# Performance work log

Measured on AMD Instinct MI355X. Metric: run time of the kernel, lower is better.

## Reference

```python
import jax, jax.numpy as jnp
import numpy as np
import math

EMB = 128
N_HEADS = 8
HEAD_DIM = EMB // N_HEADS
TANH_CLIP = 10.0
NEG_INF = -1e9


def make_heads(x, n_heads):
    # x: (B, n, H) -> (B, n_heads, n, head_dim)
    B, n, H = x.shape
    return x.reshape(B, n, n_heads, H // n_heads).transpose(0, 2, 1, 3)


def setup_inputs() -> dict:
    key = jax.random.key(0)
    ks = jax.random.split(key, 11)
    B, N, H = 64, 2000, EMB
    s = 1.0 / math.sqrt(H)
    return {
        "patch_embeddings": jax.random.normal(ks[0], (B, N, H), jnp.float32),
        "fixed_content_cls": jax.random.normal(ks[1], (B, 1, H), jnp.float32),
        "Wq_graph": jax.random.normal(ks[2], (H, H), jnp.float32) * s,
        "Wq_first": jax.random.normal(ks[3], (H, H), jnp.float32) * s,
        "Wq_last": jax.random.normal(ks[4], (H, H), jnp.float32) * s,
        "Wk": jax.random.normal(ks[5], (H, H), jnp.float32) * s,
        "Wv": jax.random.normal(ks[6], (H, H), jnp.float32) * s,
        "logit_Wk": jax.random.normal(ks[7], (H, H), jnp.float32) * s,
        "Wc": jax.random.normal(ks[8], (H, H), jnp.float32) * s,
        "bc": jax.random.normal(ks[9], (H,), jnp.float32) * s,
        "last_patch": jax.random.randint(ks[10], (B,), 0, N, jnp.int64),
    }


def reference(patch_embeddings, fixed_content_cls, Wq_graph, Wq_first, Wq_last,
              Wk, Wv, logit_Wk, Wc, bc, last_patch):
    B, N, H = patch_embeddings.shape
    bidx = jnp.arange(B)

    # reset(): precomputed projections over all patches (memory-dominant)
    q_graph = make_heads(fixed_content_cls @ Wq_graph.T, N_HEADS)   # (B, nh, 1, hd)
    glimpse_k = make_heads(patch_embeddings @ Wk.T, N_HEADS)        # (B, nh, N, hd)
    glimpse_v = make_heads(patch_embeddings @ Wv.T, N_HEADS)        # (B, nh, N, hd)
    logit_k = patch_embeddings @ logit_Wk.T                          # (B, N, H)

    # mask the just-visited patch (emulate -inf with large negative for stability)
    mask = jnp.zeros((B, N), patch_embeddings.dtype).at[bidx, last_patch].set(NEG_INF)

    # gather last patch embedding: (B, 1, H)
    last_emb = patch_embeddings[bidx, last_patch][:, None, :]
    q_first = make_heads(last_emb @ Wq_first.T, N_HEADS)
    q_last = make_heads(last_emb @ Wq_last.T, N_HEADS)
    glimpse_q = q_graph + q_first + q_last                          # (B, nh, 1, hd)

    # masked multi-head attention, q_len = 1
    scores = jnp.einsum('bhqd,bhnd->bhqn', glimpse_q, glimpse_k) / math.sqrt(HEAD_DIM)
    scores = scores + mask[:, None, None, :]
    attn = jax.nn.softmax(scores, axis=-1)
    out = jnp.einsum('bhqn,bhnd->bhqd', attn, glimpse_v)            # (B, nh, 1, hd)
    out = out.transpose(0, 2, 1, 3).reshape(B, 1, H)

    final_q = out @ Wc.T + bc                                        # (B, 1, H)

    # tanh-clipped pointer logits over all N patches
    score = jnp.einsum('bqh,bnh->bqn', final_q, logit_k) / math.sqrt(H)  # (B, 1, N)
    score_masked = TANH_CLIP * jnp.tanh(score[:, 0, :]) + mask          # (B, N)
    probs = jax.nn.softmax(score_masked, axis=1)
    return probs
```

## Files before the change

kernel.cpp:

```cpp
#include <hip/hip_runtime.h>
#include <math.h>

#define BB 64
#define NN 2000
#define HH 128
#define NHEAD 8
#define SP 8

__global__ __launch_bounds__(128) void k1_prep(
    const float* __restrict__ pe, const float* __restrict__ cls,
    const float* __restrict__ Wqg, const float* __restrict__ Wqf,
    const float* __restrict__ Wql, const float* __restrict__ Wk,
    const int* __restrict__ lp, float* __restrict__ qk_out) {
  __shared__ float4 sc4[32], sl4[32];
  __shared__ float q[HH];
  int b = blockIdx.x, t = threadIdx.x;
  int last = lp[b];
  if (t < 32) {
    sc4[t] = ((const float4*)(cls + b*HH))[t];
    sl4[t] = ((const float4*)(pe + ((long)b*NN + last)*HH))[t];
  }
  __syncthreads();
  const float4* wg = (const float4*)(Wqg + t*HH);
  const float4* wf = (const float4*)(Wqf + t*HH);
  const float4* wl = (const float4*)(Wql + t*HH);
  float acc = 0.f;
  #pragma unroll 8
  for (int j = 0; j < 32; j++) {
    float4 g = wg[j], f = wf[j], l = wl[j], c = sc4[j], s = sl4[j];
    acc += g.x*c.x + g.y*c.y + g.z*c.z + g.w*c.w;
    acc += (f.x+l.x)*s.x + (f.y+l.y)*s.y + (f.z+l.z)*s.z + (f.w+l.w)*s.w;
  }
  q[t] = acc;
  __syncthreads();
  #pragma unroll
  for (int h = 0; h < NHEAD; h++) {
    float a = 0.f;
    #pragma unroll
    for (int d = 0; d < 16; d++)
      a += q[h*16+d] * Wk[(h*16+d)*HH + t];
    qk_out[(b*NHEAD + h)*HH + t] = a * 0.25f;
  }
}

__global__ __launch_bounds__(256) void k2a_scores(
    const float* __restrict__ pe, const float* __restrict__ qk,
    const int* __restrict__ lp, float* __restrict__ pout) {
  int b = blockIdx.y, sp = blockIdx.x, tid = threadIdx.x;
  int n = sp*256 + tid;
  int nc = min(n, NN-1);
  const float4* prow = (const float4*)(pe + ((long)b*NN + nc)*HH);
  const float4* qk4  = (const float4*)(qk + (long)b*NHEAD*HH);
  float d[NHEAD];
  #pragma unroll
  for (int h = 0; h < NHEAD; h++) d[h] = 0.f;
  #pragma unroll 2
  for (int j = 0; j < 32; j += 4) {
    float4 v0 = prow[j], v1 = prow[j+1], v2 = prow[j+2], v3 = prow[j+3];
    #pragma unroll
    for (int h = 0; h < NHEAD; h++) {
      float4 q0 = qk4[h*32+j], q1 = qk4[h*32+j+1];
      float4 q2 = qk4[h*32+j+2], q3 = qk4[h*32+j+3];
      d[h] += v0.x*q0.x + v0.y*q0.y + v0.z*q0.z + v0.w*q0.w
            + v1.x*q1.x + v1.y*q1.y + v1.z*q1.z + v1.w*q1.w
            + v2.x*q2.x + v2.y*q2.y + v2.z*q2.z + v2.w*q2.w
            + v3.x*q3.x + v3.y*q3.y + v3.z*q3.z + v3.w*q3.w;
    }
  }
  int last = lp[b];
  bool live = (n < NN) && (n != last);
  float4 p0, p1;
  p0.x = live ? __expf(d[0]) : 0.f;
  p0.y = live ? __expf(d[1]) : 0.f;
  p0.z = live ? __expf(d[2]) : 0.f;
  p0.w = live ? __expf(d[3]) : 0.f;
  p1.x = live ? __expf(d[4]) : 0.f;
  p1.y = live ? __expf(d[5]) : 0.f;
  p1.z = live ? __expf(d[6]) : 0.f;
  p1.w = live ? __expf(d[7]) : 0.f;
  if (n < NN) {
    float4* po = (float4*)(pout + ((long)b*NN + n)*NHEAD);
    po[0] = p0; po[1] = p1;
  }
}

__global__ __launch_bounds__(256) void k2b_wsum(
    const float* __restrict__ pe, const float* __restrict__ pin,
    float* __restrict__ Wpart, float* __restrict__ lpart) {
  int b = blockIdx.y, sp = blockIdx.x, tid = threadIdx.x;
  int w = tid >> 6, lane = tid & 63;
  __shared__ float4 pst[4][128];
  __shared__ float4 wred[NHEAD][4][32];
  __shared__ float lred[4][NHEAD];
  int chunk = sp*256 + w*64;
  const float4* pin4 = (const float4*)pin;
  {
    float4 z = make_float4(0.f,0.f,0.f,0.f);
    int k0 = lane, k1 = lane + 64;
    int n0 = chunk + (k0 >> 1), n1 = chunk + (k1 >> 1);
    pst[w][k0] = (n0 < NN) ? pin4[((long)b*NN + n0)*2 + (k0&1)] : z;
    pst[w][k1] = (n1 < NN) ? pin4[((long)b*NN + n1)*2 + (k1&1)] : z;
  }
  __syncthreads();
  int rhalf = lane >> 5, j4 = lane & 31;
  const float4* peg = (const float4*)pe;
  float4 wa[NHEAD];
  float la[NHEAD];
  #pragma unroll
  for (int h = 0; h < NHEAD; h++) { wa[h] = make_float4(0.f,0.f,0.f,0.f); la[h] = 0.f; }
  for (int i = 0; i < 32; i++) {
    int nl = i*2 + rhalf;
    int ng = chunk + nl;
    float4 v = peg[((long)b*NN + min(ng, NN-1))*32 + j4];
    float4 pa = pst[w][nl*2], pb = pst[w][nl*2+1];
    wa[0].x += pa.x*v.x; wa[0].y += pa.x*v.y; wa[0].z += pa.x*v.z; wa[0].w += pa.x*v.w; la[0] += pa.x;
    wa[1].x += pa.y*v.x; wa[1].y += pa.y*v.y; wa[1].z += pa.y*v.z; wa[1].w += pa.y*v.w; la[1] += pa.y;
    wa[2].x += pa.z*v.x; wa[2].y += pa.z*v.y; wa[2].z += pa.z*v.z; wa[2].w += pa.z*v.w; la[2] += pa.z;
    wa[3].x += pa.w*v.x; wa[3].y += pa.w*v.y; wa[3].z += pa.w*v.z; wa[3].w += pa.w*v.w; la[3] += pa.w;
    wa[4].x += pb.x*v.x; wa[4].y += pb.x*v.y; wa[4].z += pb.x*v.z; wa[4].w += pb.x*v.w; la[4] += pb.x;
    wa[5].x += pb.y*v.x; wa[5].y += pb.y*v.y; wa[5].z += pb.y*v.z; wa[5].w += pb.y*v.w; la[5] += pb.y;
    wa[6].x += pb.z*v.x; wa[6].y += pb.z*v.y; wa[6].z += pb.z*v.z; wa[6].w += pb.z*v.w; la[6] += pb.z;
    wa[7].x += pb.w*v.x; wa[7].y += pb.w*v.y; wa[7].z += pb.w*v.z; wa[7].w += pb.w*v.w; la[7] += pb.w;
  }
  #pragma unroll
  for (int h = 0; h < NHEAD; h++) {
    wa[h].x += __shfl_xor(wa[h].x, 32);
    wa[h].y += __shfl_xor(wa[h].y, 32);
    wa[h].z += __shfl_xor(wa[h].z, 32);
    wa[h].w += __shfl_xor(wa[h].w, 32);
    la[h]   += __shfl_xor(la[h], 32);
  }
  if (lane < 32) {
    #pragma unroll
    for (int h = 0; h < NHEAD; h++) wred[h][w][lane] = wa[h];
  }
  if (lane == 0) {
    #pragma unroll
    for (int h = 0; h < NHEAD; h++) lred[w][h] = la[h];
  }
  __syncthreads();
  int h2 = tid >> 5, c = tid & 31;
  float4 s0 = wred[h2][0][c], s1 = wred[h2][1][c], s2 = wred[h2][2][c], s3 = wred[h2][3][c];
  float4 s;
  s.x = s0.x + s1.x + s2.x + s3.x;
  s.y = s0.y + s1.y + s2.y + s3.y;
  s.z = s0.z + s1.z + s2.z + s3.z;
  s.w = s0.w + s1.w + s2.w + s3.w;
  ((float4*)(Wpart + ((long)(b*SP + sp)*NHEAD + h2)*HH))[c] = s;
  if (tid < NHEAD)
    lpart[(b*SP + sp)*NHEAD + tid] =
        lred[0][tid] + lred[1][tid] + lred[2][tid] + lred[3][tid];
}

__global__ __launch_bounds__(256) void k34(
    const float* __restrict__ lpart, const float* __restrict__ Wpart,
    const float* __restrict__ Wv, const float* __restrict__ Wc,
    const float* __restrict__ bc, const float* __restrict__ lWk,
    float* __restrict__ lq_out) {
  int b = blockIdx.x, tid = threadIdx.x;
  __shared__ float Wns[NHEAD*HH];
  __shared__ float ls[NHEAD];
  __shared__ float tmp[2][HH];
  __shared__ float outf[HH], fq[HH];
  for (int e = tid; e < NHEAD*HH; e += 256) {
    float a = 0.f;
    #pragma unroll
    for (int s = 0; s < SP; s++) a += Wpart[((long)(b*SP+s)*NHEAD)*HH + e];
    Wns[e] = a;
  }
  if (tid < NHEAD) {
    float l = 0.f;
    #pragma unroll
    for (int s = 0; s < SP; s++) l += lpart[(b*SP+s)*NHEAD + tid];
    ls[tid] = l;
  }
  __syncthreads();
  int t = tid & 127, half = tid >> 7;
  {
    int h = t >> 4;
    const float4* wv = (const float4*)(Wv + t*HH);
    const float4* wn = (const float4*)(Wns + h*HH);
    float a = 0.f;
    #pragma unroll 4
    for (int j = half*16; j < half*16 + 16; j++) {
      float4 v = wv[j], nn = wn[j];
      a += v.x*nn.x + v.y*nn.y + v.z*nn.z + v.w*nn.w;
    }
    tmp[half][t] = a;
    __syncthreads();
    if (half == 0) outf[t] = (tmp[0][t] + tmp[1][t]) / ls[t>>4];
    __syncthreads();
  }
  {
    const float4* wc = (const float4*)(Wc + t*HH);
    const float4* of = (const float4*)outf;
    float a = 0.f;
    #pragma unroll 4
    for (int k = half*16; k < half*16 + 16; k++) {
      float4 v = wc[k], nn = of[k];
      a += v.x*nn.x + v.y*nn.y + v.z*nn.z + v.w*nn.w;
    }
    tmp[half][t] = a;
    __syncthreads();
    if (half == 0) fq[t] = tmp[0][t] + tmp[1][t] + bc[t];
    __syncthreads();
  }
  {
    float a = 0.f;
    #pragma unroll 4
    for (int i = half*64; i < half*64 + 64; i++)
      a += fq[i] * lWk[i*HH + t];
    tmp[half][t] = a;
    __syncthreads();
    if (half == 0)
      lq_out[b*HH + t] = (tmp[0][t] + tmp[1][t]) * 0.08838834764831845f;
  }
}

__global__ __launch_bounds__(256) void k4_logits(
    const float* __restrict__ pe, const float* __restrict__ lq,
    const int* __restrict__ lp, float* __restrict__ eout, float* __restrict__ psum) {
  int b = blockIdx.y, sp = blockIdx.x, tid = threadIdx.x;
  int n = sp*256 + tid;
  int nc = min(n, NN-1);
  const float4* prow = (const float4*)(pe + ((long)b*NN + nc)*HH);
  const float4* lq4  = (const float4*)(lq + (long)b*HH);
  float a0 = 0.f, a1 = 0.f, a2 = 0.f, a3 = 0.f;
  #pragma unroll 2
  for (int j = 0; j < 32; j += 4) {
    float4 v0 = prow[j], v1 = prow[j+1], v2 = prow[j+2], v3 = prow[j+3];
    float4 q0 = lq4[j], q1 = lq4[j+1], q2 = lq4[j+2], q3 = lq4[j+3];
    a0 += v0.x*q0.x + v0.y*q0.y + v0.z*q0.z + v0.w*q0.w;
    a1 += v1.x*q1.x + v1.y*q1.y + v1.z*q1.z + v1.w*q1.w;
    a2 += v2.x*q2.x + v2.y*q2.y + v2.z*q2.z + v2.w*q2.w;
    a3 += v3.x*q3.x + v3.y*q3.y + v3.z*q3.z + v3.w*q3.w;
  }
  float acc = (a0 + a1) + (a2 + a3);
  int last = lp[b];
  float e = (n < NN && n != last) ? __expf(-20.f / (__expf(2.f*acc) + 1.f)) : 0.f;
  if (n < NN) eout[b*NN + n] = e;
  float s = e;
  #pragma unroll
  for (int d = 1; d < 64; d <<= 1) s += __shfl_xor(s, d);
  __shared__ float red[4];
  if ((tid & 63) == 0) red[tid >> 6] = s;
  __syncthreads();
  if (tid == 0) psum[b*SP + sp] = red[0] + red[1] + red[2] + red[3];
}

__global__ __launch_bounds__(256) void k5_scale(
    const float* __restrict__ eout, const float* __restrict__ psum,
    float* __restrict__ out) {
  int b = blockIdx.y, sp = blockIdx.x, tid = threadIdx.x;
  __shared__ float S;
  if (tid == 0) {
    float a = 0.f;
    #pragma unroll
    for (int s = 0; s < SP; s++) a += psum[b*SP + s];
    S = a;
  }
  __syncthreads();
  float inv = 1.f / S;
  int lo = sp*250;
  int n = lo + tid;
  if (tid < 250) out[b*NN + n] = eout[b*NN + n] * inv;
}

extern "C" void kernel_launch(void* const* d_in, const int* in_sizes, int n_in,
                              void* d_out, int out_size, void* d_ws, size_t ws_size,
                              hipStream_t stream) {
  (void)in_sizes; (void)n_in; (void)out_size; (void)ws_size;
  const float* pe   = (const float*)d_in[0];
  const float* cls  = (const float*)d_in[1];
  const float* Wqg  = (const float*)d_in[2];
  const float* Wqf  = (const float*)d_in[3];
  const float* Wql  = (const float*)d_in[4];
  const float* Wk   = (const float*)d_in[5];
  const float* Wv   = (const float*)d_in[6];
  const float* lWk  = (const float*)d_in[7];
  const float* Wc   = (const float*)d_in[8];
  const float* bc   = (const float*)d_in[9];
  const int*   lp   = (const int*)d_in[10];
  float* out = (float*)d_out;
  float* ws  = (float*)d_ws;

  float* qk    = ws;
  float* p     = qk + BB*NHEAD*HH;
  float* lpart = p + (size_t)BB*NN*NHEAD;
  float* Wpart = lpart + BB*SP*NHEAD;
  float* lq    = Wpart + (size_t)BB*SP*NHEAD*HH;
  float* eout  = lq + BB*HH;
  float* psum  = eout + BB*NN;

  k1_prep<<<dim3(BB), dim3(128), 0, stream>>>(pe, cls, Wqg, Wqf, Wql, Wk, lp, qk);
  k2a_scores<<<dim3(SP, BB), dim3(256), 0, stream>>>(pe, qk, lp, p);
  k2b_wsum<<<dim3(SP, BB), dim3(256), 0, stream>>>(pe, p, Wpart, lpart);
  k34<<<dim3(BB), dim3(256), 0, stream>>>(lpart, Wpart, Wv, Wc, bc, lWk, lq);
  k4_logits<<<dim3(SP, BB), dim3(256), 0, stream>>>(pe, lq, lp, eout, psum);
  k5_scale<<<dim3(SP, BB), dim3(256), 0, stream>>>(eout, psum, out);
}
```

Before: 76.05 us.

## Fuse pipeline into one cooperative kernel with grid syncs and on-chip probabilities

Replaces the six separate launches with a single cooperative persistent kernel (512 blocks) that uses grid.sync between the query prep, attention score/weighted-sum, output projection, logits and normalisation phases. The attention probabilities now stay in shared memory instead of round-tripping through a global buffer, and the logit exponentials stay in registers instead of going through eout. This removes launch gaps and some global traffic, at the cost of four grid-wide barriers. Phases like query prep and the per-batch projection run on only 64 of the 512 blocks while the rest wait. A fallback multi-kernel path is kept in case cooperative launch is unavailable.

```diff
diff --git a/kernel.cpp b/kernel.cpp
--- a/kernel.cpp
+++ b/kernel.cpp
@@ -1,126 +1,114 @@
 #include <hip/hip_runtime.h>
+#include <hip/hip_cooperative_groups.h>
 #include <math.h>
+
+namespace cg = cooperative_groups;
 
 #define BB 64
 #define NN 2000
 #define HH 128
 #define NHEAD 8
 #define SP 8
-
-__global__ __launch_bounds__(128) void k1_prep(
-    const float* __restrict__ pe, const float* __restrict__ cls,
-    const float* __restrict__ Wqg, const float* __restrict__ Wqf,
-    const float* __restrict__ Wql, const float* __restrict__ Wk,
-    const int* __restrict__ lp, float* __restrict__ qk_out) {
-  __shared__ float4 sc4[32], sl4[32];
-  __shared__ float q[HH];
-  int b = blockIdx.x, t = threadIdx.x;
-  int last = lp[b];
-  if (t < 32) {
-    sc4[t] = ((const float4*)(cls + b*HH))[t];
-    sl4[t] = ((const float4*)(pe + ((long)b*NN + last)*HH))[t];
-  }
-  __syncthreads();
-  const float4* wg = (const float4*)(Wqg + t*HH);
-  const float4* wf = (const float4*)(Wqf + t*HH);
-  const float4* wl = (const float4*)(Wql + t*HH);
-  float acc = 0.f;
-  #pragma unroll 8
-  for (int j = 0; j < 32; j++) {
-    float4 g = wg[j], f = wf[j], l = wl[j], c = sc4[j], s = sl4[j];
-    acc += g.x*c.x + g.y*c.y + g.z*c.z + g.w*c.w;
-    acc += (f.x+l.x)*s.x + (f.y+l.y)*s.y + (f.z+l.z)*s.z + (f.w+l.w)*s.w;
-  }
-  q[t] = acc;
-  __syncthreads();
-  #pragma unroll
-  for (int h = 0; h < NHEAD; h++) {
-    float a = 0.f;
-    #pragma unroll
-    for (int d = 0; d < 16; d++)
-      a += q[h*16+d] * Wk[(h*16+d)*HH + t];
-    qk_out[(b*NHEAD + h)*HH + t] = a * 0.25f;
-  }
-}
-
-__global__ __launch_bounds__(256) void k2a_scores(
-    const float* __restrict__ pe, const float* __restrict__ qk,
-    const int* __restrict__ lp, float* __restrict__ pout) {
-  int b = blockIdx.y, sp = blockIdx.x, tid = threadIdx.x;
-  int n = sp*256 + tid;
-  int nc = min(n, NN-1);
-  const float4* prow = (const float4*)(pe + ((long)b*NN + nc)*HH);
-  const float4* qk4  = (const float4*)(qk + (long)b*NHEAD*HH);
-  float d[NHEAD];
-  #pragma unroll
-  for (int h = 0; h < NHEAD; h++) d[h] = 0.f;
-  #pragma unroll 2
-  for (int j = 0; j < 32; j += 4) {
-    float4 v0 = prow[j], v1 = prow[j+1], v2 = prow[j+2], v3 = prow[j+3];
+#define RPB 250
+
+#define SM_BYTES 24528
+
+
+__device__ __forceinline__ void body_qk(
+    const float* pe, const float* cls, const float* Wqg, const float* Wqf,
+    const float* Wql, const float* Wk, int b, int last, int tid,
+    float4* sc4, float4* sl4, float* qv, float* qk) {
+  if (tid < 32) {
+    sc4[tid] = ((const float4*)(cls + b*HH))[tid];
+    sl4[tid] = ((const float4*)(pe + ((long)b*NN + last)*HH))[tid];
+  }
+  __syncthreads();
+  if (tid < 128) {
+    const float4* wg = (const float4*)(Wqg + tid*HH);
+    const float4* wf = (const float4*)(Wqf + tid*HH);
+    const float4* wl = (const float4*)(Wql + tid*HH);
+    float acc = 0.f;
+    #pragma unroll 8
+    for (int j = 0; j < 32; j++) {
+      float4 g = wg[j], f = wf[j], l = wl[j], c = sc4[j], s = sl4[j];
+      acc += g.x*c.x + g.y*c.y + g.z*c.z + g.w*c.w;
+      acc += (f.x+l.x)*s.x + (f.y+l.y)*s.y + (f.z+l.z)*s.z + (f.w+l.w)*s.w;
+    }
+    qv[tid] = acc;
+  }
+  __syncthreads();
+  if (tid < 128) {
     #pragma unroll
     for (int h = 0; h < NHEAD; h++) {
-      float4 q0 = qk4[h*32+j], q1 = qk4[h*32+j+1];
-      float4 q2 = qk4[h*32+j+2], q3 = qk4[h*32+j+3];
-      d[h] += v0.x*q0.x + v0.y*q0.y + v0.z*q0.z + v0.w*q0.w
-            + v1.x*q1.x + v1.y*q1.y + v1.z*q1.z + v1.w*q1.w
-            + v2.x*q2.x + v2.y*q2.y + v2.z*q2.z + v2.w*q2.w
-            + v3.x*q3.x + v3.y*q3.y + v3.z*q3.z + v3.w*q3.w;
-    }
-  }
-  int last = lp[b];
-  bool live = (n < NN) && (n != last);
-  float4 p0, p1;
-  p0.x = live ? __expf(d[0]) : 0.f;
-  p0.y = live ? __expf(d[1]) : 0.f;
-  p0.z = live ? __expf(d[2]) : 0.f;
-  p0.w = live ? __expf(d[3]) : 0.f;
-  p1.x = live ? __expf(d[4]) : 0.f;
-  p1.y = live ? __expf(d[5]) : 0.f;
-  p1.z = live ? __expf(d[6]) : 0.f;
-  p1.w = live ? __expf(d[7]) : 0.f;
-  if (n < NN) {
-    float4* po = (float4*)(pout + ((long)b*NN + n)*NHEAD);
-    po[0] = p0; po[1] = p1;
-  }
-}
-
-__global__ __launch_bounds__(256) void k2b_wsum(
-    const float* __restrict__ pe, const float* __restrict__ pin,
-    float* __restrict__ Wpart, float* __restrict__ lpart) {
-  int b = blockIdx.y, sp = blockIdx.x, tid = threadIdx.x;
-  int w = tid >> 6, lane = tid & 63;
-  __shared__ float4 pst[4][128];
-  __shared__ float4 wred[NHEAD][4][32];
-  __shared__ float lred[4][NHEAD];
-  int chunk = sp*256 + w*64;
-  const float4* pin4 = (const float4*)pin;
-  {
-    float4 z = make_float4(0.f,0.f,0.f,0.f);
-    int k0 = lane, k1 = lane + 64;
-    int n0 = chunk + (k0 >> 1), n1 = chunk + (k1 >> 1);
-    pst[w][k0] = (n0 < NN) ? pin4[((long)b*NN + n0)*2 + (k0&1)] : z;
-    pst[w][k1] = (n1 < NN) ? pin4[((long)b*NN + n1)*2 + (k1&1)] : z;
-  }
-  __syncthreads();
-  int rhalf = lane >> 5, j4 = lane & 31;
-  const float4* peg = (const float4*)pe;
+      float a = 0.f;
+      #pragma unroll
+      for (int d = 0; d < 16; d++)
+        a += qv[h*16+d] * Wk[(h*16+d)*HH + tid];
+      qk[(b*NHEAD + h)*HH + tid] = a * 0.25f;
+    }
+  }
+}
+
+__device__ __forceinline__ void body_scores_wsum(
+    const float* pe, const float* qk, int b, int sp, int last, int tid,
+    float (*pl)[NHEAD], float4 (*wred)[4][32], float (*lred)[NHEAD],
+    float* Wpart, float* lpart) {
+  const int n0 = sp * RPB;
+  if (tid < RPB) {
+    const int n = n0 + tid;
+    const float4* prow = (const float4*)(pe + ((long)b*NN + n)*HH);
+    const float4* qk4  = (const float4*)(qk + (long)b*NHEAD*HH);
+    float d[NHEAD];
+    #pragma unroll
+    for (int h = 0; h < NHEAD; h++) d[h] = 0.f;
+    #pragma unroll 2
+    for (int j = 0; j < 32; j += 4) {
+      float4 v0 = prow[j], v1 = prow[j+1], v2 = prow[j+2], v3 = prow[j+3];
+      #pragma unroll
+      for (int h = 0; h < NHEAD; h++) {
+        float4 q0 = qk4[h*32+j],   q1 = qk4[h*32+j+1];
+        float4 q2 = qk4[h*32+j+2], q3 = qk4[h*32+j+3];
+        d[h] += v0.x*q0.x + v0.y*q0.y + v0.z*q0.z + v0.w*q0.w
+              + v1.x*q1.x + v1.y*q1.y + v1.z*q1.z + v1.w*q1.w
+              + v2.x*q2.x + v2.y*q2.y + v2.z*q2.z + v2.w*q2.w
+              + v3.x*q3.x + v3.y*q3.y + v3.z*q3.z + v3.w*q3.w;
+      }
+    }
+    const bool live = (n != last);
+    float4 p0, p1;
+    p0.x = live ? __expf(d[0]) : 0.f;  p0.y = live ? __expf(d[1]) : 0.f;
+    p0.z = live ? __expf(d[2]) : 0.f;  p0.w = live ? __expf(d[3]) : 0.f;
+    p1.x = live ? __expf(d[4]) : 0.f;  p1.y = live ? __expf(d[5]) : 0.f;
+    p1.z = live ? __expf(d[6]) : 0.f;  p1.w = live ? __expf(d[7]) : 0.f;
+    ((float4*)pl[tid])[0] = p0;
+    ((float4*)pl[tid])[1] = p1;
+  }
+  __syncthreads();
+
+  const int w = tid >> 6, lane = tid & 63;
+  const int st = w*2 + (lane >> 5);
+  const int j4 = lane & 31;
+  const float4* peg = (const float4*)(pe + ((long)b*NN + n0)*HH);
   float4 wa[NHEAD];
-  float la[NHEAD];
+  float  la[NHEAD];
   #pragma unroll
   for (int h = 0; h < NHEAD; h++) { wa[h] = make_float4(0.f,0.f,0.f,0.f); la[h] = 0.f; }
+  #pragma unroll 4
   for (int i = 0; i < 32; i++) {
-    int nl = i*2 + rhalf;
-    int ng = chunk + nl;
-    float4 v = peg[((long)b*NN + min(ng, NN-1))*32 + j4];
-    float4 pa = pst[w][nl*2], pb = pst[w][nl*2+1];
-    wa[0].x += pa.x*v.x; wa[0].y += pa.x*v.y; wa[0].z += pa.x*v.z; wa[0].w += pa.x*v.w; la[0] += pa.x;
-    wa[1].x += pa.y*v.x; wa[1].y += pa.y*v.y; wa[1].z += pa.y*v.z; wa[1].w += pa.y*v.w; la[1] += pa.y;
-    wa[2].x += pa.z*v.x; wa[2].y += pa.z*v.y; wa[2].z += pa.z*v.z; wa[2].w += pa.z*v.w; la[2] += pa.z;
-    wa[3].x += pa.w*v.x; wa[3].y += pa.w*v.y; wa[3].z += pa.w*v.z; wa[3].w += pa.w*v.w; la[3] += pa.w;
-    wa[4].x += pb.x*v.x; wa[4].y += pb.x*v.y; wa[4].z += pb.x*v.z; wa[4].w += pb.x*v.w; la[4] += pb.x;
-    wa[5].x += pb.y*v.x; wa[5].y += pb.y*v.y; wa[5].z += pb.y*v.z; wa[5].w += pb.y*v.w; la[5] += pb.y;
-    wa[6].x += pb.z*v.x; wa[6].y += pb.z*v.y; wa[6].z += pb.z*v.z; wa[6].w += pb.z*v.w; la[6] += pb.z;
-    wa[7].x += pb.w*v.x; wa[7].y += pb.w*v.y; wa[7].z += pb.w*v.z; wa[7].w += pb.w*v.w; la[7] += pb.w;
+    const int nl = st + (i << 3);
+    if (nl < RPB) {
+      float4 v  = peg[nl*32 + j4];
+      float4 pa = *(const float4*)&pl[nl][0];
+      float4 pb = *(const float4*)&pl[nl][4];
+      wa[0].x += pa.x*v.x; wa[0].y += pa.x*v.y; wa[0].z += pa.x*v.z; wa[0].w += pa.x*v.w; la[0] += pa.x;
+      wa[1].x += pa.y*v.x; wa[1].y += pa.y*v.y; wa[1].z += pa.y*v.z; wa[1].w += pa.y*v.w; la[1] += pa.y;
+      wa[2].x += pa.z*v.x; wa[2].y += pa.z*v.y; wa[2].z += pa.z*v.z; wa[2].w += pa.z*v.w; la[2] += pa.z;
+      wa[3].x += pa.w*v.x; wa[3].y += pa.w*v.y; wa[3].z += pa.w*v.z; wa[3].w += pa.w*v.w; la[3] += pa.w;
+      wa[4].x += pb.x*v.x; wa[4].y += pb.x*v.y; wa[4].z += pb.x*v.z; wa[4].w += pb.x*v.w; la[4] += pb.x;
+      wa[5].x += pb.y*v.x; wa[5].y += pb.y*v.y; wa[5].z += pb.y*v.z; wa[5].w += pb.y*v.w; la[5] += pb.y;
+      wa[6].x += pb.z*v.x; wa[6].y += pb.z*v.y; wa[6].z += pb.z*v.z; wa[6].w += pb.z*v.w; la[6] += pb.z;
+      wa[7].x += pb.w*v.x; wa[7].y += pb.w*v.y; wa[7].z += pb.w*v.z; wa[7].w += pb.w*v.w; la[7] += pb.w;
+    }
   }
   #pragma unroll
   for (int h = 0; h < NHEAD; h++) {
@@ -139,7 +127,7 @@
     for (int h = 0; h < NHEAD; h++) lred[w][h] = la[h];
   }
   __syncthreads();
-  int h2 = tid >> 5, c = tid & 31;
+  const int h2 = tid >> 5, c = tid & 31;
   float4 s0 = wred[h2][0][c], s1 = wred[h2][1][c], s2 = wred[h2][2][c], s3 = wred[h2][3][c];
   float4 s;
   s.x = s0.x + s1.x + s2.x + s3.x;
@@ -152,32 +140,27 @@
         lred[0][tid] + lred[1][tid] + lred[2][tid] + lred[3][tid];
 }
 
-__global__ __launch_bounds__(256) void k34(
-    const float* __restrict__ lpart, const float* __restrict__ Wpart,
-    const float* __restrict__ Wv, const float* __restrict__ Wc,
-    const float* __restrict__ bc, const float* __restrict__ lWk,
-    float* __restrict__ lq_out) {
-  int b = blockIdx.x, tid = threadIdx.x;
-  __shared__ float Wns[NHEAD*HH];
-  __shared__ float ls[NHEAD];
-  __shared__ float tmp[2][HH];
-  __shared__ float outf[HH], fq[HH];
+__device__ __forceinline__ void body_k34(
+    const float* lpart, const float* Wpart, const float* Wv, const float* Wc,
+    const float* bc, const float* lWk, int B2, int tid,
+    float* Wns, float* lsm, float (*tmp)[HH], float* outf, float* fq,
+    float* lq) {
   for (int e = tid; e < NHEAD*HH; e += 256) {
     float a = 0.f;
     #pragma unroll
-    for (int s = 0; s < SP; s++) a += Wpart[((long)(b*SP+s)*NHEAD)*HH + e];
+    for (int s = 0; s < SP; s++) a += Wpart[((long)(B2*SP+s)*NHEAD)*HH + e];
     Wns[e] = a;
   }
   if (tid < NHEAD) {
     float l = 0.f;
     #pragma unroll
-    for (int s = 0; s < SP; s++) l += lpart[(b*SP+s)*NHEAD + tid];
-    ls[tid] = l;
-  }
-  __syncthreads();
-  int t = tid & 127, half = tid >> 7;
+    for (int s = 0; s < SP; s++) l += lpart[(B2*SP+s)*NHEAD + tid];
+    lsm[tid] = l;
+  }
+  __syncthreads();
+  const int t = tid & 127, half = tid >> 7;
   {
-    int h = t >> 4;
+    const int h = t >> 4;
     const float4* wv = (const float4*)(Wv + t*HH);
     const float4* wn = (const float4*)(Wns + h*HH);
     float a = 0.f;
@@ -188,7 +171,7 @@
     }
     tmp[half][t] = a;
     __syncthreads();
-    if (half == 0) outf[t] = (tmp[0][t] + tmp[1][t]) / ls[t>>4];
+    if (half == 0) outf[t] = (tmp[0][t] + tmp[1][t]) / lsm[t>>4];
     __syncthreads();
   }
   {
@@ -213,17 +196,13 @@
     tmp[half][t] = a;
     __syncthreads();
     if (half == 0)
-      lq_out[b*HH + t] = (tmp[0][t] + tmp[1][t]) * 0.08838834764831845f;
-  }
-}
-
-__global__ __launch_bounds__(256) void k4_logits(
-    const float* __restrict__ pe, const float* __restrict__ lq,
-    const int* __restrict__ lp, float* __restrict__ eout, float* __restrict__ psum) {
-  int b = blockIdx.y, sp = blockIdx.x, tid = threadIdx.x;
-  int n = sp*256 + tid;
-  int nc = min(n, NN-1);
-  const float4* prow = (const float4*)(pe + ((long)b*NN + nc)*HH);
+      lq[B2*HH + t] = (tmp[0][t] + tmp[1][t]) * 0.08838834764831845f;
+  }
+}
+
+__device__ __forceinline__ float body_logit(
+    const float* pe, const float* lq, int b, int n, int last) {
+  const float4* prow = (const float4*)(pe + ((long)b*NN + n)*HH);
   const float4* lq4  = (const float4*)(lq + (long)b*HH);
   float a0 = 0.f, a1 = 0.f, a2 = 0.f, a3 = 0.f;
   #pragma unroll 2
@@ -235,20 +214,127 @@
     a2 += v2.x*q2.x + v2.y*q2.y + v2.z*q2.z + v2.w*q2.w;
     a3 += v3.x*q3.x + v3.y*q3.y + v3.z*q3.z + v3.w*q3.w;
   }
-  float acc = (a0 + a1) + (a2 + a3);
-  int last = lp[b];
-  float e = (n < NN && n != last) ? __expf(-20.f / (__expf(2.f*acc) + 1.f)) : 0.f;
-  if (n < NN) eout[b*NN + n] = e;
+  const float acc = (a0 + a1) + (a2 + a3);
+  return (n != last) ? __expf(-20.f / (__expf(2.f*acc) + 1.f)) : 0.f;
+}
+
+
+__global__ __launch_bounds__(256, 2) void mega(
+    const float* __restrict__ pe, const float* __restrict__ cls,
+    const float* __restrict__ Wqg, const float* __restrict__ Wqf,
+    const float* __restrict__ Wql, const float* __restrict__ Wk,
+    const float* __restrict__ Wv, const float* __restrict__ lWk,
+    const float* __restrict__ Wc, const float* __restrict__ bc,
+    const int* __restrict__ lp, float* __restrict__ out,
+    float* __restrict__ qk, float* __restrict__ Wpart,
+    float* __restrict__ lpart, float* __restrict__ lq,
+    float* __restrict__ psum) {
+  cg::grid_group grid = cg::this_grid();
+  const int gb = blockIdx.x;
+  const int b = gb >> 3, sp = gb & 7;
+  const int tid = threadIdx.x;
+
+  __shared__ __align__(16) char smraw[SM_BYTES];
+  float  (*pl)[NHEAD]      = reinterpret_cast<float(*)[NHEAD]>(smraw);
+  float4 (*wred)[4][32]    = reinterpret_cast<float4(*)[4][32]>(smraw + 8000);
+  float  (*lred)[NHEAD]    = reinterpret_cast<float(*)[NHEAD]>(smraw + 24384);
+  float4 *sc4              = reinterpret_cast<float4*>(smraw);
+  float4 *sl4              = reinterpret_cast<float4*>(smraw + 512);
+  float  *qv               = reinterpret_cast<float*>(smraw + 1024);
+  float  *Wns              = reinterpret_cast<float*>(smraw);
+  float  *lsm              = reinterpret_cast<float*>(smraw + 4096);
+  float  (*tmp)[HH]        = reinterpret_cast<float(*)[HH]>(smraw + 4128);
+  float  *outf             = reinterpret_cast<float*>(smraw + 5152);
+  float  *fq               = reinterpret_cast<float*>(smraw + 5664);
+  float  *red              = reinterpret_cast<float*>(smraw + 24512);
+
+  const int last = lp[b];
+
+  if (sp == 0)
+    body_qk(pe, cls, Wqg, Wqf, Wql, Wk, b, last, tid, sc4, sl4, qv, qk);
+  grid.sync();
+
+  body_scores_wsum(pe, qk, b, sp, last, tid, pl, wred, lred, Wpart, lpart);
+  grid.sync();
+
+  if (gb < BB)
+    body_k34(lpart, Wpart, Wv, Wc, bc, lWk, gb, tid, Wns, lsm, tmp, outf, fq, lq);
+  grid.sync();
+
+  const int n3 = sp*RPB + tid;
+  float e = (tid < RPB) ? body_logit(pe, lq, b, n3, last) : 0.f;
+  {
+    float s = e;
+    #pragma unroll
+    for (int d = 1; d < 64; d <<= 1) s += __shfl_xor(s, d);
+    if ((tid & 63) == 0) red[tid >> 6] = s;
+    __syncthreads();
+    if (tid == 0) psum[b*SP + sp] = red[0] + red[1] + red[2] + red[3];
+  }
+  grid.sync();
+
+  if (tid < RPB) {
+    float S = 0.f;
+    #pragma unroll
+    for (int s = 0; s < SP; s++) S += psum[b*SP + s];
+    out[b*NN + n3] = e / S;
+  }
+}
+
+
+__global__ __launch_bounds__(256) void fb_k1(
+    const float* __restrict__ pe, const float* __restrict__ cls,
+    const float* __restrict__ Wqg, const float* __restrict__ Wqf,
+    const float* __restrict__ Wql, const float* __restrict__ Wk,
+    const int* __restrict__ lp, float* __restrict__ qk) {
+  __shared__ float4 sc4[32], sl4[32];
+  __shared__ float qv[HH];
+  int b = blockIdx.x;
+  body_qk(pe, cls, Wqg, Wqf, Wql, Wk, b, lp[b], threadIdx.x, sc4, sl4, qv, qk);
+}
+
+__global__ __launch_bounds__(256) void fb_kb(
+    const float* __restrict__ pe, const float* __restrict__ qk,
+    const int* __restrict__ lp, float* __restrict__ Wpart,
+    float* __restrict__ lpart) {
+  __shared__ float  pl[RPB][NHEAD];
+  __shared__ float4 wred[NHEAD][4][32];
+  __shared__ float  lred[4][NHEAD];
+  int b = blockIdx.y, sp = blockIdx.x;
+  body_scores_wsum(pe, qk, b, sp, lp[b], threadIdx.x, pl, wred, lred, Wpart, lpart);
+}
+
+__global__ __launch_bounds__(256) void fb_k34(
+    const float* __restrict__ lpart, const float* __restrict__ Wpart,
+    const float* __restrict__ Wv, const float* __restrict__ Wc,
+    const float* __restrict__ bc, const float* __restrict__ lWk,
+    float* __restrict__ lq) {
+  __shared__ float Wns[NHEAD*HH];
+  __shared__ float lsm[NHEAD];
+  __shared__ float tmp[2][HH];
+  __shared__ float outf[HH], fq[HH];
+  body_k34(lpart, Wpart, Wv, Wc, bc, lWk, blockIdx.x, threadIdx.x,
+           Wns, lsm, tmp, outf, fq, lq);
+}
+
+__global__ __launch_bounds__(256) void fb_kd(
+    const float* __restrict__ pe, const float* __restrict__ lq,
+    const int* __restrict__ lp, float* __restrict__ eout,
+    float* __restrict__ psum) {
+  __shared__ float red[4];
+  int b = blockIdx.y, sp = blockIdx.x, tid = threadIdx.x;
+  int n = sp*RPB + tid;
+  float e = (tid < RPB) ? body_logit(pe, lq, b, n, lp[b]) : 0.f;
+  if (tid < RPB) eout[b*NN + n] = e;
   float s = e;
   #pragma unroll
   for (int d = 1; d < 64; d <<= 1) s += __shfl_xor(s, d);
-  __shared__ float red[4];
   if ((tid & 63) == 0) red[tid >> 6] = s;
   __syncthreads();
   if (tid == 0) psum[b*SP + sp] = red[0] + red[1] + red[2] + red[3];
 }
 
-__global__ __launch_bounds__(256) void k5_scale(
+__global__ __launch_bounds__(256) void fb_ke(
     const float* __restrict__ eout, const float* __restrict__ psum,
     float* __restrict__ out) {
   int b = blockIdx.y, sp = blockIdx.x, tid = threadIdx.x;
@@ -260,11 +346,10 @@
     S = a;
   }
   __syncthreads();
-  float inv = 1.f / S;
-  int lo = sp*250;
-  int n = lo + tid;
-  if (tid < 250) out[b*NN + n] = eout[b*NN + n] * inv;
-}
+  int n = sp*RPB + tid;
+  if (tid < RPB) out[b*NN + n] = eout[b*NN + n] / S;
+}
+
 
 extern "C" void kernel_launch(void* const* d_in, const int* in_sizes, int n_in,
                               void* d_out, int out_size, void* d_ws, size_t ws_size,
@@ -285,17 +370,41 @@
   float* ws  = (float*)d_ws;
 
   float* qk    = ws;
-  float* p     = qk + BB*NHEAD*HH;
-  float* lpart = p + (size_t)BB*NN*NHEAD;
-  float* Wpart = lpart + BB*SP*NHEAD;
-  float* lq    = Wpart + (size_t)BB*SP*NHEAD*HH;
-  float* eout  = lq + BB*HH;
-  float* psum  = eout + BB*NN;
-
-  k1_prep<<<dim3(BB), dim3(128), 0, stream>>>(pe, cls, Wqg, Wqf, Wql, Wk, lp, qk);
-  k2a_scores<<<dim3(SP, BB), dim3(256), 0, stream>>>(pe, qk, lp, p);
-  k2b_wsum<<<dim3(SP, BB), dim3(256), 0, stream>>>(pe, p, Wpart, lpart);
-  k34<<<dim3(BB), dim3(256), 0, stream>>>(lpart, Wpart, Wv, Wc, bc, lWk, lq);
-  k4_logits<<<dim3(SP, BB), dim3(256), 0, stream>>>(pe, lq, lp, eout, psum);
-  k5_scale<<<dim3(SP, BB), dim3(256), 0, stream>>>(eout, psum, out);
-}
+  float* Wpart = qk + BB*NHEAD*HH;
+  float* lpart = Wpart + (size_t)BB*SP*NHEAD*HH;
+  float* lq    = lpart + BB*SP*NHEAD;
+  float* psum  = lq + BB*HH;
+  float* eout  = psum + BB*SP;
+
+  bool coop_ok = false;
+  {
+    int dev = 0;
+    if (hipGetDevice(&dev) == hipSuccess) {
+      int attr = 0, ncu = 0, nb = 0;
+      hipDeviceGetAttribute(&attr, hipDeviceAttributeCooperativeLaunch, dev);
+      hipDeviceGetAttribute(&ncu, hipDeviceAttributeMultiprocessorCount, dev);
+      hipError_t oe = hipOccupancyMaxActiveBlocksPerMultiprocessor(
+          &nb, (const void*)mega, 256, 0);
+      if (attr && oe == hipSuccess && (long)nb * ncu >= (long)BB*SP)
+        coop_ok = true;
+    }
+  }
+
+  if (coop_ok) {
+    void* args[] = {
+      (void*)&pe, (void*)&cls, (void*)&Wqg, (void*)&Wqf, (void*)&Wql,
+      (void*)&Wk, (void*)&Wv, (void*)&lWk, (void*)&Wc, (void*)&bc,
+      (void*)&lp, (void*)&out, (void*)&qk, (void*)&Wpart, (void*)&lpart,
+      (void*)&lq, (void*)&psum
+    };
+    hipError_t le = hipLaunchCooperativeKernel((const void*)mega, dim3(BB*SP),
+                                               dim3(256), args, 0, stream);
+    if (le == hipSuccess) return;
+  }
+
+  fb_k1<<<dim3(BB), dim3(256), 0, stream>>>(pe, cls, Wqg, Wqf, Wql, Wk, lp, qk);
+  fb_kb<<<dim3(SP, BB), dim3(256), 0, stream>>>(pe, qk, lp, Wpart, lpart);
+  fb_k34<<<dim3(BB), dim3(256), 0, stream>>>(lpart, Wpart, Wv, Wc, bc, lWk, lq);
+  fb_kd<<<dim3(SP, BB), dim3(256), 0, stream>>>(pe, lq, lp, eout, psum);
+  fb_ke<<<dim3(SP, BB), dim3(256), 0, stream>>>(eout, psum, out);
+}
```

Measured after the change: 73.01 us. 1.04x faster.

## Fuse attention score and weighted-sum kernels, write logits directly into output

Applied to the files above, without the earlier changes.

Merges the score/exp kernel and the weighted-value-sum kernel into one block that computes exp scores for 125 rows into shared memory and then accumulates the weighted sums, so the per-head probability buffer no longer goes through global memory. Splits the q·Wk prep across (batch, head) blocks for more parallelism. The logit kernel writes unnormalised exps straight into the output and the final kernel rescales in place, which drops the eout buffer. Split count rises to 16 blocks of 125 rows each, with register-resident row loads. This means more partials to reduce and higher register pressure from the 32-float4 row arrays.

```diff
diff --git a/kernel.cpp b/kernel.cpp
--- a/kernel.cpp
+++ b/kernel.cpp
@@ -5,122 +5,112 @@
 #define NN 2000
 #define HH 128
 #define NHEAD 8
-#define SP 8
-
-__global__ __launch_bounds__(128) void k1_prep(
+#define SPB 16
+#define RPB 125
+
+__global__ __launch_bounds__(64) void k1qk(
     const float* __restrict__ pe, const float* __restrict__ cls,
     const float* __restrict__ Wqg, const float* __restrict__ Wqf,
     const float* __restrict__ Wql, const float* __restrict__ Wk,
     const int* __restrict__ lp, float* __restrict__ qk_out) {
+  const int blk = blockIdx.x, b = blk >> 3, h = blk & 7;
+  const int t = threadIdx.x;
   __shared__ float4 sc4[32], sl4[32];
-  __shared__ float q[HH];
-  int b = blockIdx.x, t = threadIdx.x;
-  int last = lp[b];
-  if (t < 32) {
-    sc4[t] = ((const float4*)(cls + b*HH))[t];
-    sl4[t] = ((const float4*)(pe + ((long)b*NN + last)*HH))[t];
-  }
-  __syncthreads();
-  const float4* wg = (const float4*)(Wqg + t*HH);
-  const float4* wf = (const float4*)(Wqf + t*HH);
-  const float4* wl = (const float4*)(Wql + t*HH);
-  float acc = 0.f;
-  #pragma unroll 8
-  for (int j = 0; j < 32; j++) {
-    float4 g = wg[j], f = wf[j], l = wl[j], c = sc4[j], s = sl4[j];
-    acc += g.x*c.x + g.y*c.y + g.z*c.z + g.w*c.w;
-    acc += (f.x+l.x)*s.x + (f.y+l.y)*s.y + (f.z+l.z)*s.z + (f.w+l.w)*s.w;
-  }
-  q[t] = acc;
-  __syncthreads();
-  #pragma unroll
-  for (int h = 0; h < NHEAD; h++) {
-    float a = 0.f;
-    #pragma unroll
-    for (int d = 0; d < 16; d++)
-      a += q[h*16+d] * Wk[(h*16+d)*HH + t];
-    qk_out[(b*NHEAD + h)*HH + t] = a * 0.25f;
-  }
-}
-
-__global__ __launch_bounds__(256) void k2a_scores(
+  __shared__ float qs[16];
+  const int last = lp[b];
+  if (t < 32) sc4[t] = ((const float4*)(cls + b*HH))[t];
+  else        sl4[t-32] = ((const float4*)(pe + ((long)b*NN + last)*HH))[t-32];
+  __syncthreads();
+  {
+    const int dot = t >> 2, part = t & 3;
+    const float4* wg = (const float4*)(Wqg + (h*16+dot)*HH) + part*8;
+    const float4* wf = (const float4*)(Wqf + (h*16+dot)*HH) + part*8;
+    const float4* wl = (const float4*)(Wql + (h*16+dot)*HH) + part*8;
+    float a = 0.f;
+    #pragma unroll
+    for (int k = 0; k < 8; k++) {
+      float4 g = wg[k], f = wf[k], l = wl[k];
+      float4 c = sc4[part*8+k], s = sl4[part*8+k];
+      a += g.x*c.x + g.y*c.y + g.z*c.z + g.w*c.w;
+      a += (f.x+l.x)*s.x + (f.y+l.y)*s.y + (f.z+l.z)*s.z + (f.w+l.w)*s.w;
+    }
+    a += __shfl_xor(a, 1);
+    a += __shfl_xor(a, 2);
+    if (part == 0) qs[dot] = a;
+  }
+  __syncthreads();
+  float v0 = 0.f, v1 = 0.f;
+  #pragma unroll
+  for (int d2 = 0; d2 < 16; d2++) {
+    const float* wkr = Wk + (h*16+d2)*HH;
+    float q = qs[d2];
+    v0 += q * wkr[t];
+    v1 += q * wkr[t+64];
+  }
+  qk_out[(b*NHEAD+h)*HH + t]      = v0 * 0.25f;
+  qk_out[(b*NHEAD+h)*HH + t + 64] = v1 * 0.25f;
+}
+
+__global__ __launch_bounds__(128) void kB(
     const float* __restrict__ pe, const float* __restrict__ qk,
-    const int* __restrict__ lp, float* __restrict__ pout) {
-  int b = blockIdx.y, sp = blockIdx.x, tid = threadIdx.x;
-  int n = sp*256 + tid;
-  int nc = min(n, NN-1);
-  const float4* prow = (const float4*)(pe + ((long)b*NN + nc)*HH);
-  const float4* qk4  = (const float4*)(qk + (long)b*NHEAD*HH);
-  float d[NHEAD];
-  #pragma unroll
-  for (int h = 0; h < NHEAD; h++) d[h] = 0.f;
-  #pragma unroll 2
-  for (int j = 0; j < 32; j += 4) {
-    float4 v0 = prow[j], v1 = prow[j+1], v2 = prow[j+2], v3 = prow[j+3];
-    #pragma unroll
-    for (int h = 0; h < NHEAD; h++) {
-      float4 q0 = qk4[h*32+j], q1 = qk4[h*32+j+1];
-      float4 q2 = qk4[h*32+j+2], q3 = qk4[h*32+j+3];
-      d[h] += v0.x*q0.x + v0.y*q0.y + v0.z*q0.z + v0.w*q0.w
-            + v1.x*q1.x + v1.y*q1.y + v1.z*q1.z + v1.w*q1.w
-            + v2.x*q2.x + v2.y*q2.y + v2.z*q2.z + v2.w*q2.w
-            + v3.x*q3.x + v3.y*q3.y + v3.z*q3.z + v3.w*q3.w;
-    }
-  }
-  int last = lp[b];
-  bool live = (n < NN) && (n != last);
-  float4 p0, p1;
-  p0.x = live ? __expf(d[0]) : 0.f;
-  p0.y = live ? __expf(d[1]) : 0.f;
-  p0.z = live ? __expf(d[2]) : 0.f;
-  p0.w = live ? __expf(d[3]) : 0.f;
-  p1.x = live ? __expf(d[4]) : 0.f;
-  p1.y = live ? __expf(d[5]) : 0.f;
-  p1.z = live ? __expf(d[6]) : 0.f;
-  p1.w = live ? __expf(d[7]) : 0.f;
-  if (n < NN) {
-    float4* po = (float4*)(pout + ((long)b*NN + n)*NHEAD);
-    po[0] = p0; po[1] = p1;
-  }
-}
-
-__global__ __launch_bounds__(256) void k2b_wsum(
-    const float* __restrict__ pe, const float* __restrict__ pin,
-    float* __restrict__ Wpart, float* __restrict__ lpart) {
-  int b = blockIdx.y, sp = blockIdx.x, tid = threadIdx.x;
-  int w = tid >> 6, lane = tid & 63;
-  __shared__ float4 pst[4][128];
-  __shared__ float4 wred[NHEAD][4][32];
-  __shared__ float lred[4][NHEAD];
-  int chunk = sp*256 + w*64;
-  const float4* pin4 = (const float4*)pin;
-  {
-    float4 z = make_float4(0.f,0.f,0.f,0.f);
-    int k0 = lane, k1 = lane + 64;
-    int n0 = chunk + (k0 >> 1), n1 = chunk + (k1 >> 1);
-    pst[w][k0] = (n0 < NN) ? pin4[((long)b*NN + n0)*2 + (k0&1)] : z;
-    pst[w][k1] = (n1 < NN) ? pin4[((long)b*NN + n1)*2 + (k1&1)] : z;
-  }
-  __syncthreads();
-  int rhalf = lane >> 5, j4 = lane & 31;
-  const float4* peg = (const float4*)pe;
+    const int* __restrict__ lp, float* __restrict__ Wpart,
+    float* __restrict__ lpart) {
+  const int b = blockIdx.y, sp = blockIdx.x, tid = threadIdx.x;
+  __shared__ float  pl[RPB][NHEAD];
+  __shared__ float4 wred[NHEAD][2][32];
+  __shared__ float  lred[2][NHEAD];
+  const int last = lp[b];
+  const int n0 = sp * RPB;
+
+  if (tid < RPB) {
+    const int n = n0 + tid;
+    const float4* prow = (const float4*)(pe + ((long)b*NN + n)*HH);
+    const float4* qk4  = (const float4*)(qk + (long)b*NHEAD*HH);
+    float4 r[32];
+    #pragma unroll
+    for (int j = 0; j < 32; j++) r[j] = prow[j];
+    float d[NHEAD];
+    #pragma unroll
+    for (int h = 0; h < NHEAD; h++) d[h] = 0.f;
+    #pragma unroll
+    for (int j = 0; j < 32; j++) {
+      const float4 v = r[j];
+      #pragma unroll
+      for (int h = 0; h < NHEAD; h++) {
+        const float4 q = qk4[h*32 + j];
+        d[h] += v.x*q.x + v.y*q.y + v.z*q.z + v.w*q.w;
+      }
+    }
+    const bool live = (n != last);
+    #pragma unroll
+    for (int h = 0; h < NHEAD; h++) pl[tid][h] = live ? __expf(d[h]) : 0.f;
+  }
+  __syncthreads();
+
+  const int w = tid >> 6, lane = tid & 63;
+  const int st = w*2 + (lane >> 5);
+  const int j4 = lane & 31;
+  const float4* peg = (const float4*)(pe + ((long)b*NN + n0)*HH);
   float4 wa[NHEAD];
-  float la[NHEAD];
+  float  la[NHEAD];
   #pragma unroll
   for (int h = 0; h < NHEAD; h++) { wa[h] = make_float4(0.f,0.f,0.f,0.f); la[h] = 0.f; }
+  #pragma unroll 4
   for (int i = 0; i < 32; i++) {
-    int nl = i*2 + rhalf;
-    int ng = chunk + nl;
-    float4 v = peg[((long)b*NN + min(ng, NN-1))*32 + j4];
-    float4 pa = pst[w][nl*2], pb = pst[w][nl*2+1];
-    wa[0].x += pa.x*v.x; wa[0].y += pa.x*v.y; wa[0].z += pa.x*v.z; wa[0].w += pa.x*v.w; la[0] += pa.x;
-    wa[1].x += pa.y*v.x; wa[1].y += pa.y*v.y; wa[1].z += pa.y*v.z; wa[1].w += pa.y*v.w; la[1] += pa.y;
-    wa[2].x += pa.z*v.x; wa[2].y += pa.z*v.y; wa[2].z += pa.z*v.z; wa[2].w += pa.z*v.w; la[2] += pa.z;
-    wa[3].x += pa.w*v.x; wa[3].y += pa.w*v.y; wa[3].z += pa.w*v.z; wa[3].w += pa.w*v.w; la[3] += pa.w;
-    wa[4].x += pb.x*v.x; wa[4].y += pb.x*v.y; wa[4].z += pb.x*v.z; wa[4].w += pb.x*v.w; la[4] += pb.x;
-    wa[5].x += pb.y*v.x; wa[5].y += pb.y*v.y; wa[5].z += pb.y*v.z; wa[5].w += pb.y*v.w; la[5] += pb.y;
-    wa[6].x += pb.z*v.x; wa[6].y += pb.z*v.y; wa[6].z += pb.z*v.z; wa[6].w += pb.z*v.w; la[6] += pb.z;
-    wa[7].x += pb.w*v.x; wa[7].y += pb.w*v.y; wa[7].z += pb.w*v.z; wa[7].w += pb.w*v.w; la[7] += pb.w;
+    const int nl = st + (i << 2);
+    if (nl < RPB) {
+      float4 v  = peg[nl*32 + j4];
+      float4 pa = *(const float4*)&pl[nl][0];
+      float4 pb = *(const float4*)&pl[nl][4];
+      wa[0].x += pa.x*v.x; wa[0].y += pa.x*v.y; wa[0].z += pa.x*v.z; wa[0].w += pa.x*v.w; la[0] += pa.x;
+      wa[1].x += pa.y*v.x; wa[1].y += pa.y*v.y; wa[1].z += pa.y*v.z; wa[1].w += pa.y*v.w; la[1] += pa.y;
+      wa[2].x += pa.z*v.x; wa[2].y += pa.z*v.y; wa[2].z += pa.z*v.z; wa[2].w += pa.z*v.w; la[2] += pa.z;
+      wa[3].x += pa.w*v.x; wa[3].y += pa.w*v.y; wa[3].z += pa.w*v.z; wa[3].w += pa.w*v.w; la[3] += pa.w;
+      wa[4].x += pb.x*v.x; wa[4].y += pb.x*v.y; wa[4].z += pb.x*v.z; wa[4].w += pb.x*v.w; la[4] += pb.x;
+      wa[5].x += pb.y*v.x; wa[5].y += pb.y*v.y; wa[5].z += pb.y*v.z; wa[5].w += pb.y*v.w; la[5] += pb.y;
+      wa[6].x += pb.z*v.x; wa[6].y += pb.z*v.y; wa[6].z += pb.z*v.z; wa[6].w += pb.z*v.w; la[6] += pb.z;
+      wa[7].x += pb.w*v.x; wa[7].y += pb.w*v.y; wa[7].z += pb.w*v.z; wa[7].w += pb.w*v.w; la[7] += pb.w;
+    }
   }
   #pragma unroll
   for (int h = 0; h < NHEAD; h++) {
@@ -139,45 +129,48 @@
     for (int h = 0; h < NHEAD; h++) lred[w][h] = la[h];
   }
   __syncthreads();
-  int h2 = tid >> 5, c = tid & 31;
-  float4 s0 = wred[h2][0][c], s1 = wred[h2][1][c], s2 = wred[h2][2][c], s3 = wred[h2][3][c];
-  float4 s;
-  s.x = s0.x + s1.x + s2.x + s3.x;
-  s.y = s0.y + s1.y + s2.y + s3.y;
-  s.z = s0.z + s1.z + s2.z + s3.z;
-  s.w = s0.w + s1.w + s2.w + s3.w;
-  ((float4*)(Wpart + ((long)(b*SP + sp)*NHEAD + h2)*HH))[c] = s;
+  {
+    const int h2 = tid >> 4, c0 = tid & 15;
+    float4* Wo = (float4*)(Wpart + ((long)(b*SPB + sp)*NHEAD + h2)*HH);
+    #pragma unroll
+    for (int k = 0; k < 2; k++) {
+      const int c = c0 + k*16;
+      float4 s0 = wred[h2][0][c], s1 = wred[h2][1][c];
+      float4 s;
+      s.x = s0.x + s1.x; s.y = s0.y + s1.y; s.z = s0.z + s1.z; s.w = s0.w + s1.w;
+      Wo[c] = s;
+    }
+  }
   if (tid < NHEAD)
-    lpart[(b*SP + sp)*NHEAD + tid] =
-        lred[0][tid] + lred[1][tid] + lred[2][tid] + lred[3][tid];
-}
-
-__global__ __launch_bounds__(256) void k34(
+    lpart[(b*SPB + sp)*NHEAD + tid] = lred[0][tid] + lred[1][tid];
+}
+
+__global__ __launch_bounds__(256) void kC(
     const float* __restrict__ lpart, const float* __restrict__ Wpart,
     const float* __restrict__ Wv, const float* __restrict__ Wc,
     const float* __restrict__ bc, const float* __restrict__ lWk,
-    float* __restrict__ lq_out) {
-  int b = blockIdx.x, tid = threadIdx.x;
+    float* __restrict__ lq) {
+  const int b = blockIdx.x, tid = threadIdx.x;
   __shared__ float Wns[NHEAD*HH];
-  __shared__ float ls[NHEAD];
+  __shared__ float lsm[NHEAD];
   __shared__ float tmp[2][HH];
   __shared__ float outf[HH], fq[HH];
   for (int e = tid; e < NHEAD*HH; e += 256) {
     float a = 0.f;
-    #pragma unroll
-    for (int s = 0; s < SP; s++) a += Wpart[((long)(b*SP+s)*NHEAD)*HH + e];
+    #pragma unroll 4
+    for (int s = 0; s < SPB; s++) a += Wpart[((long)(b*SPB+s)*NHEAD)*HH + e];
     Wns[e] = a;
   }
   if (tid < NHEAD) {
     float l = 0.f;
     #pragma unroll
-    for (int s = 0; s < SP; s++) l += lpart[(b*SP+s)*NHEAD + tid];
-    ls[tid] = l;
-  }
-  __syncthreads();
-  int t = tid & 127, half = tid >> 7;
-  {
-    int h = t >> 4;
+    for (int s = 0; s < SPB; s++) l += lpart[(b*SPB+s)*NHEAD + tid];
+    lsm[tid] = l;
+  }
+  __syncthreads();
+  const int t = tid & 127, half = tid >> 7;
+  {
+    const int h = t >> 4;
     const float4* wv = (const float4*)(Wv + t*HH);
     const float4* wn = (const float4*)(Wns + h*HH);
     float a = 0.f;
@@ -188,7 +181,7 @@
     }
     tmp[half][t] = a;
     __syncthreads();
-    if (half == 0) outf[t] = (tmp[0][t] + tmp[1][t]) / ls[t>>4];
+    if (half == 0) outf[t] = (tmp[0][t] + tmp[1][t]) / lsm[t>>4];
     __syncthreads();
   }
   {
@@ -213,57 +206,55 @@
     tmp[half][t] = a;
     __syncthreads();
     if (half == 0)
-      lq_out[b*HH + t] = (tmp[0][t] + tmp[1][t]) * 0.08838834764831845f;
-  }
-}
-
-__global__ __launch_bounds__(256) void k4_logits(
+      lq[b*HH + t] = (tmp[0][t] + tmp[1][t]) * 0.08838834764831845f;
+  }
+}
+
+__global__ __launch_bounds__(128) void kD(
     const float* __restrict__ pe, const float* __restrict__ lq,
-    const int* __restrict__ lp, float* __restrict__ eout, float* __restrict__ psum) {
-  int b = blockIdx.y, sp = blockIdx.x, tid = threadIdx.x;
-  int n = sp*256 + tid;
-  int nc = min(n, NN-1);
-  const float4* prow = (const float4*)(pe + ((long)b*NN + nc)*HH);
-  const float4* lq4  = (const float4*)(lq + (long)b*HH);
-  float a0 = 0.f, a1 = 0.f, a2 = 0.f, a3 = 0.f;
-  #pragma unroll 2
-  for (int j = 0; j < 32; j += 4) {
-    float4 v0 = prow[j], v1 = prow[j+1], v2 = prow[j+2], v3 = prow[j+3];
-    float4 q0 = lq4[j], q1 = lq4[j+1], q2 = lq4[j+2], q3 = lq4[j+3];
-    a0 += v0.x*q0.x + v0.y*q0.y + v0.z*q0.z + v0.w*q0.w;
-    a1 += v1.x*q1.x + v1.y*q1.y + v1.z*q1.z + v1.w*q1.w;
-    a2 += v2.x*q2.x + v2.y*q2.y + v2.z*q2.z + v2.w*q2.w;
-    a3 += v3.x*q3.x + v3.y*q3.y + v3.z*q3.z + v3.w*q3.w;
-  }
-  float acc = (a0 + a1) + (a2 + a3);
-  int last = lp[b];
-  float e = (n < NN && n != last) ? __expf(-20.f / (__expf(2.f*acc) + 1.f)) : 0.f;
-  if (n < NN) eout[b*NN + n] = e;
+    const int* __restrict__ lp, float* __restrict__ out,
+    float* __restrict__ psum) {
+  const int b = blockIdx.y, sp = blockIdx.x, tid = threadIdx.x;
+  __shared__ float red[2];
+  const int last = lp[b];
+  const int n = sp*RPB + tid;
+  float e = 0.f;
+  if (tid < RPB) {
+    const float4* prow = (const float4*)(pe + ((long)b*NN + n)*HH);
+    const float4* lq4  = (const float4*)(lq + (long)b*HH);
+    float4 r[32];
+    #pragma unroll
+    for (int j = 0; j < 32; j++) r[j] = prow[j];
+    float a0 = 0.f, a1 = 0.f, a2 = 0.f, a3 = 0.f;
+    #pragma unroll
+    for (int j = 0; j < 32; j += 4) {
+      float4 q0 = lq4[j], q1 = lq4[j+1], q2 = lq4[j+2], q3 = lq4[j+3];
+      a0 += r[j].x*q0.x + r[j].y*q0.y + r[j].z*q0.z + r[j].w*q0.w;
+      a1 += r[j+1].x*q1.x + r[j+1].y*q1.y + r[j+1].z*q1.z + r[j+1].w*q1.w;
+      a2 += r[j+2].x*q2.x + r[j+2].y*q2.y + r[j+2].z*q2.z + r[j+2].w*q2.w;
+      a3 += r[j+3].x*q3.x + r[j+3].y*q3.y + r[j+3].z*q3.z + r[j+3].w*q3.w;
+    }
+    const float acc = (a0 + a1) + (a2 + a3);
+    e = (n != last) ? __expf(-20.f / (__expf(2.f*acc) + 1.f)) : 0.f;
+    out[b*NN + n] = e;
+  }
   float s = e;
   #pragma unroll
   for (int d = 1; d < 64; d <<= 1) s += __shfl_xor(s, d);
-  __shared__ float red[4];
   if ((tid & 63) == 0) red[tid >> 6] = s;
   __syncthreads();
-  if (tid == 0) psum[b*SP + sp] = red[0] + red[1] + red[2] + red[3];
-}
-
-__global__ __launch_bounds__(256) void k5_scale(
-    const float* __restrict__ eout, const float* __restrict__ psum,
-    float* __restrict__ out) {
-  int b = blockIdx.y, sp = blockIdx.x, tid = threadIdx.x;
-  __shared__ float S;
-  if (tid == 0) {
-    float a = 0.f;
-    #pragma unroll
-    for (int s = 0; s < SP; s++) a += psum[b*SP + s];
-    S = a;
-  }
-  __syncthreads();
-  float inv = 1.f / S;
-  int lo = sp*250;
-  int n = lo + tid;
-  if (tid < 250) out[b*NN + n] = eout[b*NN + n] * inv;
+  if (tid == 0) psum[b*SPB + sp] = red[0] + red[1];
+}
+
+__global__ __launch_bounds__(128) void kE(
+    const float* __restrict__ psum, float* __restrict__ out) {
+  const int b = blockIdx.y, sp = blockIdx.x, tid = threadIdx.x;
+  float S = 0.f;
+  #pragma unroll
+  for (int s = 0; s < SPB; s++) S += psum[b*SPB + s];
+  const float inv = 1.f / S;
+  const int n = sp*RPB + tid;
+  if (tid < RPB) out[b*NN + n] *= inv;
 }
 
 extern "C" void kernel_launch(void* const* d_in, const int* in_sizes, int n_in,
@@ -285,17 +276,14 @@
   float* ws  = (float*)d_ws;
 
   float* qk    = ws;
-  float* p     = qk + BB*NHEAD*HH;
-  float* lpart = p + (size_t)BB*NN*NHEAD;
-  float* Wpart = lpart + BB*SP*NHEAD;
-  float* lq    = Wpart + (size_t)BB*SP*NHEAD*HH;
-  float* eout  = lq + BB*HH;
-  float* psum  = eout + BB*NN;
-
-  k1_prep<<<dim3(BB), dim3(128), 0, stream>>>(pe, cls, Wqg, Wqf, Wql, Wk, lp, qk);
-  k2a_scores<<<dim3(SP, BB), dim3(256), 0, stream>>>(pe, qk, lp, p);
-  k2b_wsum<<<dim3(SP, BB), dim3(256), 0, stream>>>(pe, p, Wpart, lpart);
-  k34<<<dim3(BB), dim3(256), 0, stream>>>(lpart, Wpart, Wv, Wc, bc, lWk, lq);
-  k4_logits<<<dim3(SP, BB), dim3(256), 0, stream>>>(pe, lq, lp, eout, psum);
-  k5_scale<<<dim3(SP, BB), dim3(256), 0, stream>>>(eout, psum, out);
-}
+  float* Wpart = qk + BB*NHEAD*HH;
+  float* lpart = Wpart + (size_t)BB*SPB*NHEAD*HH;
+  float* lq    = lpart + BB*SPB*NHEAD;
+  float* psum  = lq + BB*HH;
+
+  k1qk<<<dim3(BB*NHEAD), dim3(64), 0, stream>>>(pe, cls, Wqg, Wqf, Wql, Wk, lp, qk);
+  kB<<<dim3(SPB, BB), dim3(128), 0, stream>>>(pe, qk, lp, Wpart, lpart);
+  kC<<<dim3(BB), dim3(256), 0, stream>>>(lpart, Wpart, Wv, Wc, bc, lWk, lq);
+  kD<<<dim3(SPB, BB), dim3(128), 0, stream>>>(pe, lq, lp, out, psum);
+  kE<<<dim3(SPB, BB), dim3(128), 0, stream>>>(psum, out);
+}
```

Result: faster. 68.76 us (-9.6%).
